# Kernel tuning notes

Measured on AMD Instinct MI355X. Metric: run time of the kernel, lower is better.

The kernel has to match this reference:

```python
import jax, jax.numpy as jnp
import numpy as np

D_EMB = 256
SCALE = 0.02
B, T = 4, 4096
EPS = 1e-5


def layer_norm(x, w, b):
    m = jnp.mean(x, axis=-1, keepdims=True)
    v = jnp.mean((x - m) ** 2, axis=-1, keepdims=True)
    return (x - m) * jax.lax.rsqrt(v + EPS) * w + b


def setup_inputs() -> dict:
    key = jax.random.key(0)
    ks = jax.random.split(key, 4)
    x = jax.random.normal(ks[0], (B, T, D_EMB), dtype=jnp.float32)
    qkv = jax.random.normal(ks[1], (3, D_EMB, D_EMB), dtype=jnp.float32) * SCALE
    # nn.Linear(D, 2D, bias=False): weight shape (2D, D), applied as x @ W.T
    w1 = jax.random.normal(ks[2], (2 * D_EMB, D_EMB), dtype=jnp.float32) * (1.0 / np.sqrt(D_EMB))
    w2 = jax.random.normal(ks[3], (D_EMB, 2 * D_EMB), dtype=jnp.float32) * (1.0 / np.sqrt(2 * D_EMB))
    ones = jnp.ones((D_EMB,), dtype=jnp.float32)
    zeros = jnp.zeros((D_EMB,), dtype=jnp.float32)
    return {
        "x": x, "qkv": qkv,
        "ln_q_w": ones, "ln_q_b": zeros,
        "ln_k_w": ones, "ln_k_b": zeros,
        "ln_attn_w": ones, "ln_attn_b": zeros,
        "w1": w1, "w2": w2,
        "ln_ff_w": ones, "ln_ff_b": zeros,
    }


def reference(x, qkv, ln_q_w, ln_q_b, ln_k_w, ln_k_b, ln_attn_w, ln_attn_b, w1, w2, ln_ff_w, ln_ff_b):
    # QKV projections: [3, B, T, D]
    y = jnp.einsum('btd,ndD->nbtD', x, qkv)
    q, k, v = y[0], y[1], y[2]
    q = layer_norm(q, ln_q_w, ln_q_b)
    k = layer_norm(k, ln_k_w, ln_k_b)
    # full (non-causal) single-head attention, scale by sqrt(D_EMB)
    scores = jnp.einsum('btd,bsd->bts', q, k) / jnp.sqrt(jnp.float32(D_EMB))
    attn = jax.nn.softmax(scores, axis=-1)
    y = jnp.einsum('bts,bsd->btd', attn, v)
    y = layer_norm(y, ln_attn_w, ln_attn_b)
    x = 0.7 * (x + y)
    # FFN with dual leaky_relu
    y = jax.nn.leaky_relu(x @ w1.T, negative_slope=0.2)
    y = jax.nn.leaky_relu(y @ w2.T, negative_slope=0.2)
    y = layer_norm(y, ln_ff_w, ln_ff_b)
    return 0.7 * (x + y)
```

## Files before the change

### kernel.cpp

```cpp
#include <hip/hip_runtime.h>

#define BSZ   4
#define TSEQ  4096
#define DEMB  256
#define NTOK  (BSZ * TSEQ)
#define HID   512
#define SPLITS 4
#define KEYS_PER_SPLIT (TSEQ / SPLITS)
#define TK 32
#define NT (KEYS_PER_SPLIT / TK)
#define KIMG_STRIDE 8704
#define VIMG_STRIDE 10240

using bf16x8 = __attribute__((ext_vector_type(8))) short;
using f32x16 = __attribute__((ext_vector_type(16))) float;

static __device__ __forceinline__ unsigned short f2bf(float f) {
  union { float f; unsigned u; } v; v.f = f;
  unsigned r = v.u + 0x7FFF + ((v.u >> 16) & 1);
  return (unsigned short)(r >> 16);
}
static __device__ __forceinline__ float bf2f(unsigned short u) {
  union { unsigned u; float f; } v; v.u = ((unsigned)u) << 16;
  return v.f;
}

static __device__ __forceinline__ void async16(void* lds, const void* gp) {
  __builtin_amdgcn_global_load_lds(
      (const __attribute__((address_space(1))) unsigned int*)gp,
      (__attribute__((address_space(3))) unsigned int*)lds, 16, 0, 0);
}

__global__ __launch_bounds__(256) void prep_kernel(
    const float* __restrict__ qkv, const float* __restrict__ w1,
    const float* __restrict__ w2, unsigned short* __restrict__ qkvT,
    unsigned short* __restrict__ w1b, unsigned short* __restrict__ w2b)
{
  const int tid = threadIdx.x;
  if (blockIdx.y < 3) {
    if (blockIdx.x >= 16) return;
    __shared__ float Ts[64][65];
    const int z  = blockIdx.y;
    const int k0 = (blockIdx.x >> 2) * 64;
    const int j0 = (blockIdx.x & 3) * 64;
    const float* src = qkv + (size_t)z * DEMB * DEMB + (size_t)k0 * DEMB + j0;
#pragma unroll
    for (int p = 0; p < 4; ++p) {
      int idx = p * 256 + tid;
      int r = idx >> 4, g = idx & 15;
      float4 v = *(const float4*)(src + (size_t)r * DEMB + g * 4);
      Ts[r][g * 4 + 0] = v.x; Ts[r][g * 4 + 1] = v.y;
      Ts[r][g * 4 + 2] = v.z; Ts[r][g * 4 + 3] = v.w;
    }
    __syncthreads();
    unsigned short* dst = qkvT + (size_t)z * DEMB * DEMB + (size_t)j0 * DEMB + k0;
#pragma unroll
    for (int p = 0; p < 4; ++p) {
      int idx = p * 256 + tid;
      int r = idx >> 4, g = idx & 15;
      ushort4 o;
      o.x = f2bf(Ts[g * 4 + 0][r]); o.y = f2bf(Ts[g * 4 + 1][r]);
      o.z = f2bf(Ts[g * 4 + 2][r]); o.w = f2bf(Ts[g * 4 + 3][r]);
      *(ushort4*)(dst + (size_t)r * DEMB + g * 4) = o;
    }
  } else {
    const float* s = (blockIdx.y == 3) ? w1 : w2;
    unsigned short* d = (blockIdx.y == 3) ? w1b : w2b;
    const int i = blockIdx.x * 256 + tid;
    float4 v = ((const float4*)s)[i];
    ushort4 o;
    o.x = f2bf(v.x); o.y = f2bf(v.y); o.z = f2bf(v.z); o.w = f2bf(v.w);
    ((ushort4*)d)[i] = o;
  }
}

__global__ __launch_bounds__(512, 1) void qkvln_kernel(
    const float* __restrict__ x, const unsigned short* __restrict__ qkvT,
    const float* __restrict__ lnqw, const float* __restrict__ lnqb,
    const float* __restrict__ lnkw, const float* __restrict__ lnkb,
    unsigned short* __restrict__ Qbn, unsigned short* __restrict__ Kimg,
    unsigned short* __restrict__ Vimg)
{
  __shared__ __align__(16) unsigned short sh[36864];
  unsigned short* As = sh;
  unsigned short* Bs = sh + 256 * 72;

  const int tid = threadIdx.x;
  const int w   = tid >> 6;
  const int l   = tid & 63;
  const int lm  = l & 31;
  const int lh  = l >> 5;
  const int z   = blockIdx.y;
  const int m0  = blockIdx.x * 256;
  const int bb  = m0 >> 12;

  const unsigned short* Bt = qkvT + (size_t)z * DEMB * DEMB;

  f32x16 o[8];
#pragma unroll
  for (int t = 0; t < 8; ++t)
#pragma unroll
    for (int r = 0; r < 16; ++r) o[t][r] = 0.f;

  const int fr = tid >> 4;
  const int fc = (tid & 15) * 4;

  float4 arf[8];
  bf16x8 brb[4];

#pragma unroll
  for (int i = 0; i < 8; ++i)
    arf[i] = *(const float4*)(x + (size_t)(m0 + fr + 32 * i) * DEMB + fc);
#pragma unroll
  for (int i = 0; i < 4; ++i) {
    const int c = tid + 512 * i;
    brb[i] = *(const bf16x8*)(Bt + (size_t)(c >> 3) * DEMB + (c & 7) * 8);
  }

  for (int k0 = 0; k0 < DEMB; k0 += 64) {
    __syncthreads();
#pragma unroll
    for (int i = 0; i < 8; ++i) {
      ushort4 u;
      u.x = f2bf(arf[i].x); u.y = f2bf(arf[i].y);
      u.z = f2bf(arf[i].z); u.w = f2bf(arf[i].w);
      *(ushort4*)&As[(fr + 32 * i) * 72 + fc] = u;
    }
#pragma unroll
    for (int i = 0; i < 4; ++i) {
      const int c = tid + 512 * i;
      *(bf16x8*)&Bs[(c >> 3) * 72 + (c & 7) * 8] = brb[i];
    }
    __syncthreads();

    if (k0 + 64 < DEMB) {
      const int kn = k0 + 64;
#pragma unroll
      for (int i = 0; i < 8; ++i)
        arf[i] = *(const float4*)(x + (size_t)(m0 + fr + 32 * i) * DEMB + kn + fc);
#pragma unroll
      for (int i = 0; i < 4; ++i) {
        const int c = tid + 512 * i;
        brb[i] = *(const bf16x8*)(Bt + (size_t)(c >> 3) * DEMB + kn + (c & 7) * 8);
      }
    }

#pragma unroll
    for (int ks = 0; ks < 4; ++ks) {
      bf16x8 a = *(const bf16x8*)&As[(w * 32 + lm) * 72 + ks * 16 + lh * 8];
#pragma unroll
      for (int t = 0; t < 8; ++t) {
        bf16x8 b = *(const bf16x8*)&Bs[(t * 32 + lm) * 72 + ks * 16 + lh * 8];
        o[t] = __builtin_amdgcn_mfma_f32_32x32x16_bf16(a, b, o[t], 0, 0, 0);
      }
    }
  }

  __syncthreads();

  if (z < 2) {
    const float* wp = z ? lnkw : lnqw;
    const float* bp = z ? lnkb : lnqb;
    float wc[8], bc[8];
#pragma unroll
    for (int t = 0; t < 8; ++t) { wc[t] = wp[t * 32 + lm]; bc[t] = bp[t * 32 + lm]; }
#pragma unroll
    for (int r = 0; r < 16; ++r) {
      float sv = 0.f, sq = 0.f;
#pragma unroll
      for (int t = 0; t < 8; ++t) { const float v = o[t][r]; sv += v; sq += v * v; }
#pragma unroll
      for (int d = 1; d < 32; d <<= 1) { sv += __shfl_xor(sv, d, 64); sq += __shfl_xor(sq, d, 64); }
      const float mean = sv * (1.f / DEMB);
      const float rs = rsqrtf(sq * (1.f / DEMB) - mean * mean + 1e-5f);
      const int token = m0 + w * 32 + (r & 3) + 8 * (r >> 2) + 4 * lh;
      if (z == 0) {
        unsigned short* dst = Qbn + (size_t)token * DEMB;
#pragma unroll
        for (int t = 0; t < 8; ++t)
          dst[t * 32 + lm] = f2bf((o[t][r] - mean) * rs * wc[t] + bc[t]);
      } else {
        const int t5 = token & 4095;
        unsigned short* dst =
            Kimg + (size_t)(bb * 128 + (t5 >> 5)) * KIMG_STRIDE + (t5 & 31) * 264;
#pragma unroll
        for (int t = 0; t < 8; ++t)
          dst[t * 32 + lm] = f2bf((o[t][r] - mean) * rs * wc[t] + bc[t]);
      }
    }
  } else {
#pragma unroll
    for (int h = 0; h < 2; ++h) {
      if (h) __syncthreads();
#pragma unroll
      for (int t2 = 0; t2 < 4; ++t2) {
        const int t = h * 4 + t2;
#pragma unroll
        for (int r = 0; r < 16; ++r) {
          const int row = w * 32 + (r & 3) + 8 * (r >> 2) + 4 * lh;
          sh[row * 130 + t2 * 32 + lm] = f2bf(o[t][r]);
        }
      }
      __syncthreads();
      const int d2 = tid & 127;
      const int tq = tid >> 7;
      const int d  = h * 128 + d2;
#pragma unroll
      for (int j = 0; j < 16; ++j) {
        const int tok0 = tq * 64 + j * 4;
        ushort4 v;
        v.x = sh[(tok0 + 0) * 130 + d2];
        v.y = sh[(tok0 + 1) * 130 + d2];
        v.z = sh[(tok0 + 2) * 130 + d2];
        v.w = sh[(tok0 + 3) * 130 + d2];
        const int gtok = m0 + tok0;
        const int kt = (gtok & 4095) >> 5;
        *(ushort4*)(Vimg + (size_t)(bb * 128 + kt) * VIMG_STRIDE + d * 40 + (tok0 & 31)) = v;
      }
    }
  }
}

__global__ __launch_bounds__(256, 3) void gemm_ffn_kernel(
    const unsigned short* __restrict__ A, const unsigned short* __restrict__ Bt,
    unsigned short* __restrict__ C, int M, int N, int K)
{
  __shared__ __align__(16) unsigned short As[128 * 72];
  __shared__ __align__(16) unsigned short Bs[128 * 72];

  const int tid = threadIdx.x;
  const int w   = tid >> 6;
  const int wm  = w >> 1, wn = w & 1;
  const int l   = tid & 63;
  const int lm  = l & 31;
  const int lh  = l >> 5;

  const int m0    = blockIdx.x * 128;
  const int nbase = blockIdx.y * 128;

  f32x16 acc00, acc01, acc10, acc11;
#pragma unroll
  for (int r = 0; r < 16; ++r) { acc00[r] = 0.f; acc01[r] = 0.f; acc10[r] = 0.f; acc11[r] = 0.f; }

  const int lr = tid >> 3;
  const int lc = (tid & 7) * 8;

  bf16x8 arb[4], brb[4];

#pragma unroll
  for (int i = 0; i < 4; ++i) {
    arb[i] = *(const bf16x8*)(A  + (size_t)(m0 + i * 32 + lr) * K + lc);
    brb[i] = *(const bf16x8*)(Bt + (size_t)(nbase + i * 32 + lr) * K + lc);
  }

  for (int k0 = 0; k0 < K; k0 += 64) {
    __syncthreads();
#pragma unroll
    for (int i = 0; i < 4; ++i) {
      *(bf16x8*)&As[(i * 32 + lr) * 72 + lc] = arb[i];
      *(bf16x8*)&Bs[(i * 32 + lr) * 72 + lc] = brb[i];
    }
    __syncthreads();

    if (k0 + 64 < K) {
      const int kn = k0 + 64;
#pragma unroll
      for (int i = 0; i < 4; ++i) {
        arb[i] = *(const bf16x8*)(A  + (size_t)(m0 + i * 32 + lr) * K + kn + lc);
        brb[i] = *(const bf16x8*)(Bt + (size_t)(nbase + i * 32 + lr) * K + kn + lc);
      }
    }

#pragma unroll
    for (int ks = 0; ks < 4; ++ks) {
      bf16x8 a0 = *(const bf16x8*)&As[(wm * 64 + lm)      * 72 + ks * 16 + lh * 8];
      bf16x8 a1 = *(const bf16x8*)&As[(wm * 64 + 32 + lm) * 72 + ks * 16 + lh * 8];
      bf16x8 b0 = *(const bf16x8*)&Bs[(wn * 64 + lm)      * 72 + ks * 16 + lh * 8];
      bf16x8 b1 = *(const bf16x8*)&Bs[(wn * 64 + 32 + lm) * 72 + ks * 16 + lh * 8];
      acc00 = __builtin_amdgcn_mfma_f32_32x32x16_bf16(a0, b0, acc00, 0, 0, 0);
      acc01 = __builtin_amdgcn_mfma_f32_32x32x16_bf16(a0, b1, acc01, 0, 0, 0);
      acc10 = __builtin_amdgcn_mfma_f32_32x32x16_bf16(a1, b0, acc10, 0, 0, 0);
      acc11 = __builtin_amdgcn_mfma_f32_32x32x16_bf16(a1, b1, acc11, 0, 0, 0);
    }
  }

  const f32x16* accs[4] = { &acc00, &acc01, &acc10, &acc11 };
#pragma unroll
  for (int am = 0; am < 2; ++am)
#pragma unroll
    for (int bn = 0; bn < 2; ++bn) {
      const f32x16& a = *accs[am * 2 + bn];
#pragma unroll
      for (int r = 0; r < 16; ++r) {
        const int m = m0 + wm * 64 + am * 32 + (r & 3) + 8 * (r >> 2) + 4 * lh;
        const int n = nbase + wn * 64 + bn * 32 + lm;
        float v = a[r];
        v = v > 0.f ? v : 0.2f * v;
        C[(size_t)m * N + n] = f2bf(v);
      }
    }
}

__global__ __launch_bounds__(256) void ln_res_bf16_kernel(
    const unsigned short* __restrict__ Y, const float* __restrict__ Xin,
    const float* __restrict__ w, const float* __restrict__ b,
    float* __restrict__ Out)
{
  const int lane = threadIdx.x & 63;
  const size_t row = (size_t)blockIdx.x * 4 + (threadIdx.x >> 6);
  ushort4 u = *(const ushort4*)&Y[row * DEMB + lane * 4];
  float y0 = bf2f(u.x), y1 = bf2f(u.y), y2 = bf2f(u.z), y3 = bf2f(u.w);
  float s  = y0 + y1 + y2 + y3;
  float sq = y0 * y0 + y1 * y1 + y2 * y2 + y3 * y3;
#pragma unroll
  for (int o = 32; o > 0; o >>= 1) { s += __shfl_down(s, o); sq += __shfl_down(sq, o); }
  s = __shfl(s, 0); sq = __shfl(sq, 0);
  const float m  = s * (1.f / DEMB);
  const float rs = rsqrtf(sq * (1.f / DEMB) - m * m + 1e-5f);
  const float4 wv = *(const float4*)&w[lane * 4];
  const float4 bv = *(const float4*)&b[lane * 4];
  const float4 xi = *(const float4*)&Xin[row * DEMB + lane * 4];
  float4 o;
  o.x = 0.7f * (xi.x + (y0 - m) * rs * wv.x + bv.x);
  o.y = 0.7f * (xi.y + (y1 - m) * rs * wv.y + bv.y);
  o.z = 0.7f * (xi.z + (y2 - m) * rs * wv.z + bv.z);
  o.w = 0.7f * (xi.w + (y3 - m) * rs * wv.w + bv.w);
  *(float4*)&Out[row * DEMB + lane * 4] = o;
}

__global__ __launch_bounds__(512) void attn_split_kernel(
    const unsigned short* __restrict__ Qb, const unsigned short* __restrict__ Kimg,
    const unsigned short* __restrict__ Vimg, unsigned short* __restrict__ Opart,
    float* __restrict__ lpart)
{
  __shared__ __align__(16) unsigned short Ks[2][KIMG_STRIDE];
  __shared__ __align__(16) unsigned short Vs[3][VIMG_STRIDE];
  __shared__ __align__(16) unsigned short Pb[8 * 32 * 40];

  const int tid = threadIdx.x;
  const int w   = tid >> 6;
  const int l   = tid & 63;
  const int lm  = l & 31;
  const int lh  = l >> 5;

  const int lin = blockIdx.x;
  const int xcd = lin & 7;
  const int idx = lin >> 3;
  const int b     = xcd >> 1;
  const int split = (xcd & 1) * 2 + (idx & 1);
  const int q0    = (idx >> 1) * 256;

  const unsigned short* Qbase  = Qb + (size_t)b * TSEQ * DEMB;
  const unsigned short* Ktiles = Kimg + (size_t)(b * 128 + split * 32) * KIMG_STRIDE;
  const unsigned short* Vtiles = Vimg + (size_t)(b * 128 + split * 32) * VIMG_STRIDE;

  bf16x8 qf[16];
  {
    const unsigned short* qrow = Qbase + (size_t)(q0 + w * 32 + lm) * DEMB + lh * 8;
#pragma unroll
    for (int ks = 0; ks < 16; ++ks) qf[ks] = *(const bf16x8*)(qrow + ks * 16);
  }

  f32x16 o[8];
  float lsum[16], spv[16];
#pragma unroll
  for (int t = 0; t < 8; ++t)
#pragma unroll
    for (int r = 0; r < 16; ++r) o[t][r] = 0.f;
#pragma unroll
  for (int r = 0; r < 16; ++r) lsum[r] = 0.f;

  unsigned short* Pw = &Pb[w * 32 * 40];

#pragma unroll
  for (int i = 0; i < 3; ++i) {
    const int c = w + 8 * i;
    if (c < 17) async16(&Ks[0][c * 512], Ktiles + c * 512 + l * 8);
  }
#pragma unroll
  for (int i = 0; i < 3; ++i) {
    const int c = w + 8 * i;
    if (c < 20) async16(&Vs[0][c * 512], Vtiles + c * 512 + l * 8);
  }

  {
    __syncthreads();
#pragma unroll
    for (int i = 0; i < 3; ++i) {
      const int c = w + 8 * i;
      if (c < 17) async16(&Ks[1][c * 512], Ktiles + (size_t)KIMG_STRIDE + c * 512 + l * 8);
    }
#pragma unroll
    for (int i = 0; i < 3; ++i) {
      const int c = w + 8 * i;
      if (c < 20) async16(&Vs[1][c * 512], Vtiles + (size_t)VIMG_STRIDE + c * 512 + l * 8);
    }
    f32x16 s;
#pragma unroll
    for (int r = 0; r < 16; ++r) s[r] = 0.f;
#pragma unroll
    for (int ks = 0; ks < 16; ++ks) {
      bf16x8 kf = *(const bf16x8*)&Ks[0][lm * 264 + ks * 16 + lh * 8];
      s = __builtin_amdgcn_mfma_f32_32x32x16_bf16(qf[ks], kf, s, 0, 0, 0);
    }
#pragma unroll
    for (int r = 0; r < 16; ++r) spv[r] = s[r];
  }

  int vprev = 0, vcur = 1, vnext = 2;

  for (int st = 1; st < NT; ++st) {
    __syncthreads();

    if (st + 1 < NT) {
      const unsigned short* kn = Ktiles + (size_t)(st + 1) * KIMG_STRIDE;
      const unsigned short* vn = Vtiles + (size_t)(st + 1) * VIMG_STRIDE;
#pragma unroll
      for (int i = 0; i < 3; ++i) {
        const int c = w + 8 * i;
        if (c < 17) async16(&Ks[(st + 1) & 1][c * 512], kn + c * 512 + l * 8);
      }
#pragma unroll
      for (int i = 0; i < 3; ++i) {
        const int c = w + 8 * i;
        if (c < 20) async16(&Vs[vnext][c * 512], vn + c * 512 + l * 8);
      }
    }

#pragma unroll
    for (int r = 0; r < 16; ++r) {
      const float pv = exp2f(spv[r] * 0.09016844335f - 11.541560327f);
      lsum[r] += pv;
      const int row = (r & 3) + ((r >> 2) << 3) + (lh << 2);
      Pw[row * 40 + lm] = f2bf(pv);
    }
    {
      const unsigned short* Vp = &Vs[vprev][0];
#pragma unroll
      for (int ks = 0; ks < 2; ++ks) {
        bf16x8 pf = *(const bf16x8*)&Pw[lm * 40 + ks * 16 + lh * 8];
#pragma unroll
        for (int t = 0; t < 8; ++t) {
          bf16x8 vf = *(const bf16x8*)&Vp[(t * 32 + lm) * 40 + ks * 16 + lh * 8];
          o[t] = __builtin_amdgcn_mfma_f32_32x32x16_bf16(pf, vf, o[t], 0, 0, 0);
        }
      }
    }

    {
      f32x16 s;
#pragma unroll
      for (int r = 0; r < 16; ++r) s[r] = 0.f;
      const unsigned short* Kp = &Ks[st & 1][0];
#pragma unroll
      for (int ks = 0; ks < 16; ++ks) {
        bf16x8 kf = *(const bf16x8*)&Kp[lm * 264 + ks * 16 + lh * 8];
        s = __builtin_amdgcn_mfma_f32_32x32x16_bf16(qf[ks], kf, s, 0, 0, 0);
      }
#pragma unroll
      for (int r = 0; r < 16; ++r) spv[r] = s[r];
    }

    const int tmp = vprev; vprev = vcur; vcur = vnext; vnext = tmp;
  }

#pragma unroll
  for (int r = 0; r < 16; ++r) {
    const float pv = exp2f(spv[r] * 0.09016844335f - 11.541560327f);
    lsum[r] += pv;
    const int row = (r & 3) + ((r >> 2) << 3) + (lh << 2);
    Pw[row * 40 + lm] = f2bf(pv);
  }
  {
    const unsigned short* Vp = &Vs[vprev][0];
#pragma unroll
    for (int ks = 0; ks < 2; ++ks) {
      bf16x8 pf = *(const bf16x8*)&Pw[lm * 40 + ks * 16 + lh * 8];
#pragma unroll
      for (int t = 0; t < 8; ++t) {
        bf16x8 vf = *(const bf16x8*)&Vp[(t * 32 + lm) * 40 + ks * 16 + lh * 8];
        o[t] = __builtin_amdgcn_mfma_f32_32x32x16_bf16(pf, vf, o[t], 0, 0, 0);
      }
    }
  }

#pragma unroll
  for (int r = 0; r < 16; ++r) {
#pragma unroll
    for (int d = 1; d < 32; d <<= 1) lsum[r] += __shfl_xor(lsum[r], d, 64);
  }
  unsigned short* Ob =
      Opart + ((size_t)split * NTOK + (size_t)b * TSEQ + q0 + w * 32) * DEMB;
  float* lb = lpart + (size_t)split * NTOK + (size_t)b * TSEQ + q0 + w * 32;
#pragma unroll
  for (int r = 0; r < 16; ++r) {
    const int row = (r & 3) + ((r >> 2) << 3) + (lh << 2);
#pragma unroll
    for (int t = 0; t < 8; ++t)
      Ob[(size_t)row * DEMB + t * 32 + lm] = f2bf(o[t][r]);
    if (lm == 0) lb[row] = lsum[r];
  }
}

__global__ __launch_bounds__(256) void combine_lnres_kernel(
    const unsigned short* __restrict__ Opart, const float* __restrict__ lpart,
    const float* __restrict__ Xin, const float* __restrict__ w,
    const float* __restrict__ b, float* __restrict__ Out,
    unsigned short* __restrict__ Outb)
{
  const int lane = threadIdx.x & 63;
  const size_t row = (size_t)blockIdx.x * 4 + (threadIdx.x >> 6);
  float4 acc = make_float4(0.f, 0.f, 0.f, 0.f);
  float lt = 0.f;
#pragma unroll
  for (int p = 0; p < SPLITS; ++p) {
    const ushort4 u = *(const ushort4*)&Opart[((size_t)p * NTOK + row) * DEMB + lane * 4];
    acc.x += bf2f(u.x); acc.y += bf2f(u.y);
    acc.z += bf2f(u.z); acc.w += bf2f(u.w);
    lt += lpart[(size_t)p * NTOK + row];
  }
  const float inv = 1.f / lt;
  const float y0 = acc.x * inv, y1 = acc.y * inv, y2 = acc.z * inv, y3 = acc.w * inv;
  float s  = y0 + y1 + y2 + y3;
  float sq = y0 * y0 + y1 * y1 + y2 * y2 + y3 * y3;
#pragma unroll
  for (int o = 32; o > 0; o >>= 1) { s += __shfl_down(s, o); sq += __shfl_down(sq, o); }
  s = __shfl(s, 0); sq = __shfl(sq, 0);
  const float m  = s * (1.f / DEMB);
  const float rs = rsqrtf(sq * (1.f / DEMB) - m * m + 1e-5f);
  const float4 wv = *(const float4*)&w[lane * 4];
  const float4 bv = *(const float4*)&b[lane * 4];
  const float4 xi = *(const float4*)&Xin[row * DEMB + lane * 4];
  float4 o;
  o.x = 0.7f * (xi.x + (y0 - m) * rs * wv.x + bv.x);
  o.y = 0.7f * (xi.y + (y1 - m) * rs * wv.y + bv.y);
  o.z = 0.7f * (xi.z + (y2 - m) * rs * wv.z + bv.z);
  o.w = 0.7f * (xi.w + (y3 - m) * rs * wv.w + bv.w);
  *(float4*)&Out[row * DEMB + lane * 4] = o;
  ushort4 ob;
  ob.x = f2bf(o.x); ob.y = f2bf(o.y); ob.z = f2bf(o.z); ob.w = f2bf(o.w);
  *(ushort4*)&Outb[row * DEMB + lane * 4] = ob;
}

extern "C" void kernel_launch(void* const* d_in, const int* in_sizes, int n_in,
                              void* d_out, int out_size, void* d_ws, size_t ws_size,
                              hipStream_t stream)
{
  (void)in_sizes; (void)n_in; (void)out_size; (void)ws_size;
  const float* x    = (const float*)d_in[0];
  const float* qkv  = (const float*)d_in[1];
  const float* lnqw = (const float*)d_in[2];
  const float* lnqb = (const float*)d_in[3];
  const float* lnkw = (const float*)d_in[4];
  const float* lnkb = (const float*)d_in[5];
  const float* lnaw = (const float*)d_in[6];
  const float* lnab = (const float*)d_in[7];
  const float* w1   = (const float*)d_in[8];
  const float* w2   = (const float*)d_in[9];
  const float* lnfw = (const float*)d_in[10];
  const float* lnfb = (const float*)d_in[11];
  float* out = (float*)d_out;

  char* W = (char*)d_ws;
  const size_t MB = 1 << 20;
  unsigned short* Qbn   = (unsigned short*)(W + 0);
  unsigned short* Kimg  = (unsigned short*)(W + 8 * MB);
  unsigned short* Vimg  = (unsigned short*)(W + 17 * MB);
  unsigned short* Opart = (unsigned short*)(W + 28 * MB);
  float*          lpart = (float*)(W + 60 * MB);
  unsigned short* x1b   = (unsigned short*)(W + 0);
  unsigned short* H     = (unsigned short*)(W + 8 * MB);
  unsigned short* Y2b   = (unsigned short*)(W + 28 * MB);
  unsigned short* qkvT  = (unsigned short*)(W + 60 * MB + 512 * 1024);
  unsigned short* w1b   = (unsigned short*)(W + 61 * MB);
  unsigned short* w2b   = (unsigned short*)(W + 61 * MB + 256 * 1024);

  const dim3 blk(256);

  prep_kernel<<<dim3(128, 5), blk, 0, stream>>>(qkv, w1, w2, qkvT, w1b, w2b);

  qkvln_kernel<<<dim3(NTOK / 256, 3), dim3(512), 0, stream>>>(
      x, qkvT, lnqw, lnqb, lnkw, lnkb, Qbn, Kimg, Vimg);

  attn_split_kernel<<<dim3(256), dim3(512), 0, stream>>>(Qbn, Kimg, Vimg, Opart, lpart);
  combine_lnres_kernel<<<NTOK / 4, blk, 0, stream>>>(Opart, lpart, x, lnaw, lnab, out, x1b);

  gemm_ffn_kernel<<<dim3(NTOK / 128, HID / 128), blk, 0, stream>>>(
      x1b, w1b, H, NTOK, HID, DEMB);
  gemm_ffn_kernel<<<dim3(NTOK / 128, DEMB / 128), blk, 0, stream>>>(
      H, w2b, Y2b, NTOK, DEMB, HID);

  ln_res_bf16_kernel<<<NTOK / 4, blk, 0, stream>>>(Y2b, out, lnfw, lnfb, out);
}
```

Before: 228.0 us.

## Fuse FFN GEMMs and final layernorm into one kernel; retile QKV kernel

Replaces the two FFN GEMM launches and the separate layernorm-residual kernel with one kernel per 64-token tile. The kernel computes the hidden activations into shared memory, runs the second GEMM from there, and applies layernorm and the residual in registers. This removes the global-memory round trips for the hidden and output intermediates, plus two launches. The cost is heavy LDS use with one block per CU and every block re-reading the full weight matrices. The QKV projection kernel is also retiled to 128-token, 256-thread blocks with two blocks per CU.

```diff
diff --git a/kernel.cpp b/kernel.cpp
--- a/kernel.cpp
+++ b/kernel.cpp
@@ -74,16 +74,16 @@
   }
 }
 
-__global__ __launch_bounds__(512, 1) void qkvln_kernel(
+__global__ __launch_bounds__(256, 2) void qkvln_kernel(
     const float* __restrict__ x, const unsigned short* __restrict__ qkvT,
     const float* __restrict__ lnqw, const float* __restrict__ lnqb,
     const float* __restrict__ lnkw, const float* __restrict__ lnkb,
     unsigned short* __restrict__ Qbn, unsigned short* __restrict__ Kimg,
     unsigned short* __restrict__ Vimg)
 {
-  __shared__ __align__(16) unsigned short sh[36864];
+  __shared__ __align__(16) unsigned short sh[128 * 72 + 256 * 72];
   unsigned short* As = sh;
-  unsigned short* Bs = sh + 256 * 72;
+  unsigned short* Bs = sh + 128 * 72;
 
   const int tid = threadIdx.x;
   const int w   = tid >> 6;
@@ -91,7 +91,7 @@
   const int lm  = l & 31;
   const int lh  = l >> 5;
   const int z   = blockIdx.y;
-  const int m0  = blockIdx.x * 256;
+  const int m0  = blockIdx.x * 128;
   const int bb  = m0 >> 12;
 
   const unsigned short* Bt = qkvT + (size_t)z * DEMB * DEMB;
@@ -102,46 +102,35 @@
 #pragma unroll
     for (int r = 0; r < 16; ++r) o[t][r] = 0.f;
 
-  const int fr = tid >> 4;
-  const int fc = (tid & 15) * 4;
-
   float4 arf[8];
-  bf16x8 brb[4];
-
-#pragma unroll
-  for (int i = 0; i < 8; ++i)
-    arf[i] = *(const float4*)(x + (size_t)(m0 + fr + 32 * i) * DEMB + fc);
-#pragma unroll
-  for (int i = 0; i < 4; ++i) {
-    const int c = tid + 512 * i;
-    brb[i] = *(const bf16x8*)(Bt + (size_t)(c >> 3) * DEMB + (c & 7) * 8);
+  bf16x8 brb[8];
+#pragma unroll
+  for (int i = 0; i < 8; ++i) {
+    const int ia = i * 256 + tid;
+    arf[i] = *(const float4*)(x + (size_t)(m0 + (ia >> 4)) * DEMB + (ia & 15) * 4);
+    brb[i] = *(const bf16x8*)(Bt + (size_t)(ia >> 3) * DEMB + (ia & 7) * 8);
   }
 
   for (int k0 = 0; k0 < DEMB; k0 += 64) {
     __syncthreads();
 #pragma unroll
     for (int i = 0; i < 8; ++i) {
+      const int ia = i * 256 + tid;
       ushort4 u;
       u.x = f2bf(arf[i].x); u.y = f2bf(arf[i].y);
       u.z = f2bf(arf[i].z); u.w = f2bf(arf[i].w);
-      *(ushort4*)&As[(fr + 32 * i) * 72 + fc] = u;
-    }
-#pragma unroll
-    for (int i = 0; i < 4; ++i) {
-      const int c = tid + 512 * i;
-      *(bf16x8*)&Bs[(c >> 3) * 72 + (c & 7) * 8] = brb[i];
+      *(ushort4*)&As[(ia >> 4) * 72 + (ia & 15) * 4] = u;
+      *(bf16x8*)&Bs[(ia >> 3) * 72 + (ia & 7) * 8] = brb[i];
     }
     __syncthreads();
 
     if (k0 + 64 < DEMB) {
       const int kn = k0 + 64;
 #pragma unroll
-      for (int i = 0; i < 8; ++i)
-        arf[i] = *(const float4*)(x + (size_t)(m0 + fr + 32 * i) * DEMB + kn + fc);
-#pragma unroll
-      for (int i = 0; i < 4; ++i) {
-        const int c = tid + 512 * i;
-        brb[i] = *(const bf16x8*)(Bt + (size_t)(c >> 3) * DEMB + kn + (c & 7) * 8);
+      for (int i = 0; i < 8; ++i) {
+        const int ia = i * 256 + tid;
+        arf[i] = *(const float4*)(x + (size_t)(m0 + (ia >> 4)) * DEMB + kn + (ia & 15) * 4);
+        brb[i] = *(const bf16x8*)(Bt + (size_t)(ia >> 3) * DEMB + kn + (ia & 7) * 8);
       }
     }
 
@@ -155,8 +144,6 @@
       }
     }
   }
-
-  __syncthreads();
 
   if (z < 2) {
     const float* wp = z ? lnkw : lnqw;
@@ -191,7 +178,7 @@
   } else {
 #pragma unroll
     for (int h = 0; h < 2; ++h) {
-      if (h) __syncthreads();
+      __syncthreads();
 #pragma unroll
       for (int t2 = 0; t2 < 4; ++t2) {
         const int t = h * 4 + t2;
@@ -221,111 +208,177 @@
   }
 }
 
-__global__ __launch_bounds__(256, 3) void gemm_ffn_kernel(
-    const unsigned short* __restrict__ A, const unsigned short* __restrict__ Bt,
-    unsigned short* __restrict__ C, int M, int N, int K)
+__global__ __launch_bounds__(256, 1) void ffn_fused_kernel(
+    const unsigned short* __restrict__ x1b, const unsigned short* __restrict__ w1b,
+    const unsigned short* __restrict__ w2b, const float* __restrict__ lnw,
+    const float* __restrict__ lnb, float* __restrict__ Out)
 {
-  __shared__ __align__(16) unsigned short As[128 * 72];
-  __shared__ __align__(16) unsigned short Bs[128 * 72];
+  __shared__ __align__(16) unsigned short As[64 * 72];
+  __shared__ __align__(16) unsigned short Bs[512 * 72];
+  __shared__ __align__(16) unsigned short Hs[64 * 520];
 
   const int tid = threadIdx.x;
   const int w   = tid >> 6;
-  const int wm  = w >> 1, wn = w & 1;
   const int l   = tid & 63;
   const int lm  = l & 31;
   const int lh  = l >> 5;
-
-  const int m0    = blockIdx.x * 128;
-  const int nbase = blockIdx.y * 128;
-
-  f32x16 acc00, acc01, acc10, acc11;
-#pragma unroll
-  for (int r = 0; r < 16; ++r) { acc00[r] = 0.f; acc01[r] = 0.f; acc10[r] = 0.f; acc11[r] = 0.f; }
-
-  const int lr = tid >> 3;
-  const int lc = (tid & 7) * 8;
-
-  bf16x8 arb[4], brb[4];
-
-#pragma unroll
-  for (int i = 0; i < 4; ++i) {
-    arb[i] = *(const bf16x8*)(A  + (size_t)(m0 + i * 32 + lr) * K + lc);
-    brb[i] = *(const bf16x8*)(Bt + (size_t)(nbase + i * 32 + lr) * K + lc);
-  }
-
-  for (int k0 = 0; k0 < K; k0 += 64) {
-    __syncthreads();
-#pragma unroll
-    for (int i = 0; i < 4; ++i) {
-      *(bf16x8*)&As[(i * 32 + lr) * 72 + lc] = arb[i];
-      *(bf16x8*)&Bs[(i * 32 + lr) * 72 + lc] = brb[i];
-    }
-    __syncthreads();
-
-    if (k0 + 64 < K) {
-      const int kn = k0 + 64;
-#pragma unroll
-      for (int i = 0; i < 4; ++i) {
-        arb[i] = *(const bf16x8*)(A  + (size_t)(m0 + i * 32 + lr) * K + kn + lc);
-        brb[i] = *(const bf16x8*)(Bt + (size_t)(nbase + i * 32 + lr) * K + kn + lc);
+  const int m0  = blockIdx.x * 64;
+
+  f32x16 a1[8];
+#pragma unroll
+  for (int i = 0; i < 8; ++i)
+#pragma unroll
+    for (int r = 0; r < 16; ++r) a1[i][r] = 0.f;
+
+  bf16x8 ar[2], br[16];
+#pragma unroll
+  for (int i = 0; i < 2; ++i) {
+    const int ia = i * 256 + tid;
+    ar[i] = *(const bf16x8*)(x1b + (size_t)(m0 + (ia >> 3)) * DEMB + (ia & 7) * 8);
+  }
+#pragma unroll
+  for (int i = 0; i < 16; ++i) {
+    const int ia = i * 256 + tid;
+    br[i] = *(const bf16x8*)(w1b + (size_t)(ia >> 3) * DEMB + (ia & 7) * 8);
+  }
+
+  for (int kc = 0; kc < 4; ++kc) {
+    __syncthreads();
+#pragma unroll
+    for (int i = 0; i < 2; ++i) {
+      const int ia = i * 256 + tid;
+      *(bf16x8*)&As[(ia >> 3) * 72 + (ia & 7) * 8] = ar[i];
+    }
+#pragma unroll
+    for (int i = 0; i < 16; ++i) {
+      const int ia = i * 256 + tid;
+      *(bf16x8*)&Bs[(ia >> 3) * 72 + (ia & 7) * 8] = br[i];
+    }
+    __syncthreads();
+
+    if (kc < 3) {
+      const int kn = (kc + 1) * 64;
+#pragma unroll
+      for (int i = 0; i < 2; ++i) {
+        const int ia = i * 256 + tid;
+        ar[i] = *(const bf16x8*)(x1b + (size_t)(m0 + (ia >> 3)) * DEMB + kn + (ia & 7) * 8);
+      }
+#pragma unroll
+      for (int i = 0; i < 16; ++i) {
+        const int ia = i * 256 + tid;
+        br[i] = *(const bf16x8*)(w1b + (size_t)(ia >> 3) * DEMB + kn + (ia & 7) * 8);
       }
     }
 
 #pragma unroll
     for (int ks = 0; ks < 4; ++ks) {
-      bf16x8 a0 = *(const bf16x8*)&As[(wm * 64 + lm)      * 72 + ks * 16 + lh * 8];
-      bf16x8 a1 = *(const bf16x8*)&As[(wm * 64 + 32 + lm) * 72 + ks * 16 + lh * 8];
-      bf16x8 b0 = *(const bf16x8*)&Bs[(wn * 64 + lm)      * 72 + ks * 16 + lh * 8];
-      bf16x8 b1 = *(const bf16x8*)&Bs[(wn * 64 + 32 + lm) * 72 + ks * 16 + lh * 8];
-      acc00 = __builtin_amdgcn_mfma_f32_32x32x16_bf16(a0, b0, acc00, 0, 0, 0);
-      acc01 = __builtin_amdgcn_mfma_f32_32x32x16_bf16(a0, b1, acc01, 0, 0, 0);
-      acc10 = __builtin_amdgcn_mfma_f32_32x32x16_bf16(a1, b0, acc10, 0, 0, 0);
-      acc11 = __builtin_amdgcn_mfma_f32_32x32x16_bf16(a1, b1, acc11, 0, 0, 0);
-    }
-  }
-
-  const f32x16* accs[4] = { &acc00, &acc01, &acc10, &acc11 };
-#pragma unroll
-  for (int am = 0; am < 2; ++am)
-#pragma unroll
-    for (int bn = 0; bn < 2; ++bn) {
-      const f32x16& a = *accs[am * 2 + bn];
+      bf16x8 a0  = *(const bf16x8*)&As[lm * 72 + ks * 16 + lh * 8];
+      bf16x8 a1f = *(const bf16x8*)&As[(32 + lm) * 72 + ks * 16 + lh * 8];
+#pragma unroll
+      for (int c = 0; c < 4; ++c) {
+        bf16x8 b = *(const bf16x8*)&Bs[(w * 128 + c * 32 + lm) * 72 + ks * 16 + lh * 8];
+        a1[c * 2 + 0] = __builtin_amdgcn_mfma_f32_32x32x16_bf16(a0,  b, a1[c * 2 + 0], 0, 0, 0);
+        a1[c * 2 + 1] = __builtin_amdgcn_mfma_f32_32x32x16_bf16(a1f, b, a1[c * 2 + 1], 0, 0, 0);
+      }
+    }
+  }
+
+#pragma unroll
+  for (int c = 0; c < 4; ++c)
+#pragma unroll
+    for (int rt = 0; rt < 2; ++rt)
 #pragma unroll
       for (int r = 0; r < 16; ++r) {
-        const int m = m0 + wm * 64 + am * 32 + (r & 3) + 8 * (r >> 2) + 4 * lh;
-        const int n = nbase + wn * 64 + bn * 32 + lm;
-        float v = a[r];
+        const int row = rt * 32 + (r & 3) + 8 * (r >> 2) + 4 * lh;
+        const int col = w * 128 + c * 32 + lm;
+        float v = a1[c * 2 + rt][r];
         v = v > 0.f ? v : 0.2f * v;
-        C[(size_t)m * N + n] = f2bf(v);
-      }
-    }
-}
-
-__global__ __launch_bounds__(256) void ln_res_bf16_kernel(
-    const unsigned short* __restrict__ Y, const float* __restrict__ Xin,
-    const float* __restrict__ w, const float* __restrict__ b,
-    float* __restrict__ Out)
-{
-  const int lane = threadIdx.x & 63;
-  const size_t row = (size_t)blockIdx.x * 4 + (threadIdx.x >> 6);
-  ushort4 u = *(const ushort4*)&Y[row * DEMB + lane * 4];
-  float y0 = bf2f(u.x), y1 = bf2f(u.y), y2 = bf2f(u.z), y3 = bf2f(u.w);
-  float s  = y0 + y1 + y2 + y3;
-  float sq = y0 * y0 + y1 * y1 + y2 * y2 + y3 * y3;
-#pragma unroll
-  for (int o = 32; o > 0; o >>= 1) { s += __shfl_down(s, o); sq += __shfl_down(sq, o); }
-  s = __shfl(s, 0); sq = __shfl(sq, 0);
-  const float m  = s * (1.f / DEMB);
-  const float rs = rsqrtf(sq * (1.f / DEMB) - m * m + 1e-5f);
-  const float4 wv = *(const float4*)&w[lane * 4];
-  const float4 bv = *(const float4*)&b[lane * 4];
-  const float4 xi = *(const float4*)&Xin[row * DEMB + lane * 4];
-  float4 o;
-  o.x = 0.7f * (xi.x + (y0 - m) * rs * wv.x + bv.x);
-  o.y = 0.7f * (xi.y + (y1 - m) * rs * wv.y + bv.y);
-  o.z = 0.7f * (xi.z + (y2 - m) * rs * wv.z + bv.z);
-  o.w = 0.7f * (xi.w + (y3 - m) * rs * wv.w + bv.w);
-  *(float4*)&Out[row * DEMB + lane * 4] = o;
+        Hs[row * 520 + col] = f2bf(v);
+      }
+
+  f32x16 a2[4];
+#pragma unroll
+  for (int i = 0; i < 4; ++i)
+#pragma unroll
+    for (int r = 0; r < 16; ++r) a2[i][r] = 0.f;
+
+  bf16x8 wr[8];
+#pragma unroll
+  for (int i = 0; i < 8; ++i) {
+    const int ia = i * 256 + tid;
+    wr[i] = *(const bf16x8*)(w2b + (size_t)(ia >> 3) * HID + (ia & 7) * 8);
+  }
+
+  for (int kc = 0; kc < 8; ++kc) {
+    __syncthreads();
+#pragma unroll
+    for (int i = 0; i < 8; ++i) {
+      const int ia = i * 256 + tid;
+      *(bf16x8*)&Bs[(ia >> 3) * 72 + (ia & 7) * 8] = wr[i];
+    }
+    __syncthreads();
+
+    if (kc < 7) {
+      const int kn = (kc + 1) * 64;
+#pragma unroll
+      for (int i = 0; i < 8; ++i) {
+        const int ia = i * 256 + tid;
+        wr[i] = *(const bf16x8*)(w2b + (size_t)(ia >> 3) * HID + kn + (ia & 7) * 8);
+      }
+    }
+
+#pragma unroll
+    for (int ks = 0; ks < 4; ++ks) {
+      const int kk = kc * 64 + ks * 16 + lh * 8;
+      bf16x8 h0 = *(const bf16x8*)&Hs[lm * 520 + kk];
+      bf16x8 h1 = *(const bf16x8*)&Hs[(32 + lm) * 520 + kk];
+      bf16x8 b0 = *(const bf16x8*)&Bs[(w * 64 + lm) * 72 + ks * 16 + lh * 8];
+      bf16x8 b1 = *(const bf16x8*)&Bs[(w * 64 + 32 + lm) * 72 + ks * 16 + lh * 8];
+      a2[0] = __builtin_amdgcn_mfma_f32_32x32x16_bf16(h0, b0, a2[0], 0, 0, 0);
+      a2[1] = __builtin_amdgcn_mfma_f32_32x32x16_bf16(h1, b0, a2[1], 0, 0, 0);
+      a2[2] = __builtin_amdgcn_mfma_f32_32x32x16_bf16(h0, b1, a2[2], 0, 0, 0);
+      a2[3] = __builtin_amdgcn_mfma_f32_32x32x16_bf16(h1, b1, a2[3], 0, 0, 0);
+    }
+  }
+
+  float* Sst = (float*)As;
+#pragma unroll
+  for (int rt = 0; rt < 2; ++rt)
+#pragma unroll
+    for (int r = 0; r < 16; ++r) {
+      float y0 = a2[rt][r];      y0 = y0 > 0.f ? y0 : 0.2f * y0;
+      float y1 = a2[2 + rt][r];  y1 = y1 > 0.f ? y1 : 0.2f * y1;
+      a2[rt][r] = y0; a2[2 + rt][r] = y1;
+      float sv = y0 + y1, sq = y0 * y0 + y1 * y1;
+#pragma unroll
+      for (int d = 1; d < 32; d <<= 1) { sv += __shfl_xor(sv, d, 64); sq += __shfl_xor(sq, d, 64); }
+      const int row = rt * 32 + (r & 3) + 8 * (r >> 2) + 4 * lh;
+      if (lm == 0) { Sst[(w * 64 + row) * 2] = sv; Sst[(w * 64 + row) * 2 + 1] = sq; }
+    }
+  __syncthreads();
+  float lw[2], lb[2];
+#pragma unroll
+  for (int ct = 0; ct < 2; ++ct) {
+    lw[ct] = lnw[w * 64 + ct * 32 + lm];
+    lb[ct] = lnb[w * 64 + ct * 32 + lm];
+  }
+#pragma unroll
+  for (int rt = 0; rt < 2; ++rt)
+#pragma unroll
+    for (int r = 0; r < 16; ++r) {
+      const int row = rt * 32 + (r & 3) + 8 * (r >> 2) + 4 * lh;
+      float sv = Sst[row * 2] + Sst[(64 + row) * 2] + Sst[(128 + row) * 2] + Sst[(192 + row) * 2];
+      float sq = Sst[row * 2 + 1] + Sst[(64 + row) * 2 + 1] + Sst[(128 + row) * 2 + 1] + Sst[(192 + row) * 2 + 1];
+      const float mean = sv * (1.f / DEMB);
+      const float rs = rsqrtf(sq * (1.f / DEMB) - mean * mean + 1e-5f);
+#pragma unroll
+      for (int ct = 0; ct < 2; ++ct) {
+        const int col = w * 64 + ct * 32 + lm;
+        const float val = (a2[ct * 2 + rt][r] - mean) * rs * lw[ct] + lb[ct];
+        const size_t g = (size_t)(m0 + row) * DEMB + col;
+        Out[g] = 0.7f * (Out[g] + val);
+      }
+    }
 }
 
 __global__ __launch_bounds__(512) void attn_split_kernel(
@@ -569,8 +622,6 @@
   unsigned short* Opart = (unsigned short*)(W + 28 * MB);
   float*          lpart = (float*)(W + 60 * MB);
   unsigned short* x1b   = (unsigned short*)(W + 0);
-  unsigned short* H     = (unsigned short*)(W + 8 * MB);
-  unsigned short* Y2b   = (unsigned short*)(W + 28 * MB);
   unsigned short* qkvT  = (unsigned short*)(W + 60 * MB + 512 * 1024);
   unsigned short* w1b   = (unsigned short*)(W + 61 * MB);
   unsigned short* w2b   = (unsigned short*)(W + 61 * MB + 256 * 1024);
@@ -579,16 +630,12 @@
 
   prep_kernel<<<dim3(128, 5), blk, 0, stream>>>(qkv, w1, w2, qkvT, w1b, w2b);
 
-  qkvln_kernel<<<dim3(NTOK / 256, 3), dim3(512), 0, stream>>>(
+  qkvln_kernel<<<dim3(NTOK / 128, 3), blk, 0, stream>>>(
       x, qkvT, lnqw, lnqb, lnkw, lnkb, Qbn, Kimg, Vimg);
 
   attn_split_kernel<<<dim3(256), dim3(512), 0, stream>>>(Qbn, Kimg, Vimg, Opart, lpart);
   combine_lnres_kernel<<<NTOK / 4, blk, 0, stream>>>(Opart, lpart, x, lnaw, lnab, out, x1b);
 
-  gemm_ffn_kernel<<<dim3(NTOK / 128, HID / 128), blk, 0, stream>>>(
-      x1b, w1b, H, NTOK, HID, DEMB);
-  gemm_ffn_kernel<<<dim3(NTOK / 128, DEMB / 128), blk, 0, stream>>>(
-      H, w2b, Y2b, NTOK, DEMB, HID);
-
-  ln_res_bf16_kernel<<<NTOK / 4, blk, 0, stream>>>(Y2b, out, lnfw, lnfb, out);
-}
+  ffn_fused_kernel<<<dim3(NTOK / 64), blk, 0, stream>>>(
+      x1b, w1b, w2b, lnfw, lnfb, out);
+}
```

Result: slower. 237.4 us (+4.1%).
